# Performance work log

Hardware: AMD Instinct MI355X
Metric: run time of the kernel (lower is better)

## Reference

```python
import jax, jax.numpy as jnp
import numpy as np

K = 3  # three_nn
EPS = 1e-10


def setup_inputs() -> dict:
    key = jax.random.key(0)
    ks = jax.random.split(key, 10)
    B, N, NP = 4, 16384, 4096
    C1, C2 = 128, 256
    Cin, H1, H2, Cout = C1 + C2, 256, 256, 128
    xyz1 = jax.random.normal(ks[0], (B, N, 3), dtype=jnp.float32)
    xyz2 = jax.random.normal(ks[1], (B, NP, 3), dtype=jnp.float32)
    features1 = jax.random.normal(ks[2], (B, N, C1), dtype=jnp.float32)
    features2 = jax.random.normal(ks[3], (B, NP, C2), dtype=jnp.float32)
    def lin(k, fan_in, fan_out):
        bound = 1.0 / np.sqrt(fan_in)
        kw, kb = jax.random.split(k)
        W = jax.random.uniform(kw, (fan_in, fan_out), jnp.float32, -bound, bound)
        b = jax.random.uniform(kb, (fan_out,), jnp.float32, -bound, bound)
        return W, b
    W1, b1 = lin(ks[4], Cin, H1)
    W2, b2 = lin(ks[5], H1, H2)
    W3, b3 = lin(ks[6], H2, Cout)
    return {"xyz1": xyz1, "xyz2": xyz2, "features1": features1,
            "features2": features2, "W1": W1, "b1": b1, "W2": W2,
            "b2": b2, "W3": W3, "b3": b3}


def _three_nn(xyz1, xyz2):
    # squared pairwise distances via |a|^2 + |b|^2 - 2 a.b  -> [B, N, npoint]
    sq1 = jnp.sum(xyz1 * xyz1, axis=-1)  # [B, N]
    sq2 = jnp.sum(xyz2 * xyz2, axis=-1)  # [B, npoint]
    dots = jnp.einsum("bnd,bmd->bnm", xyz1, xyz2)
    sqdist = sq1[:, :, None] + sq2[:, None, :] - 2.0 * dots
    neg_d, idx = jax.lax.top_k(-sqdist, K)  # 3 smallest squared distances
    return -neg_d, idx  # dist:[B,N,3], idx:[B,N,3]


def reference(xyz1, xyz2, features1, features2, W1, b1, W2, b2, W3, b3):
    B = xyz1.shape[0]
    dist, idx = _three_nn(xyz1, xyz2)
    # torch custom three_nn is non-differentiable in dist
    dist = jax.lax.stop_gradient(dist)
    dist = jnp.maximum(dist, EPS)
    recip = 1.0 / dist                                  # [B, N, 3]
    weight = recip / jnp.sum(recip, axis=-1, keepdims=True)
    # three_interpolate: gather neighbor features and weighted-sum
    batch_idx = jnp.arange(B)[:, None, None]
    gathered = features2[batch_idx, idx]                # [B, N, 3, C2]
    interp = jnp.einsum("bnkc,bnk->bnc", gathered, weight)
    new_features = jnp.concatenate([features1, interp], axis=-1)
    h = jax.nn.relu(new_features @ W1 + b1)
    h = jax.nn.relu(h @ W2 + b2)
    return h @ W3 + b3
```

## Files before the change

kernel.cpp:

```cpp
#include <hip/hip_runtime.h>
#include <stdint.h>

#define QT   65536
#define NPTS 4096
#define C1   128
#define C2   256
#define CIN  384
#define COUT 128

typedef _Float16 f16;
typedef __attribute__((ext_vector_type(8))) _Float16 f16x8;
typedef __attribute__((ext_vector_type(4))) float f32x4;

__device__ __attribute__((aligned(16))) f16 g_w1p[12 * 16 * 64 * 8];
__device__ __attribute__((aligned(16))) f16 g_w2p[8 * 16 * 64 * 8];
__device__ __attribute__((aligned(16))) f16 g_w3p[8 * 8 * 64 * 8];

__device__ inline void packW(const float* __restrict__ W, f16* __restrict__ dst,
                             int i, int N, int NCB) {
  const int r = i & 63;
  const int cbk = i >> 6;
  const int cb = cbk % NCB, kcb = cbk / NCB;
  const int col = cb * 16 + (r & 15);
  const int k0 = kcb * 32 + (r >> 4) * 8;
  f16* o = dst + (size_t)i * 8;
#pragma unroll
  for (int e = 0; e < 8; ++e) o[e] = (f16)W[(size_t)(k0 + e) * N + col];
}

__global__ __launch_bounds__(256) void prep(
    const float* __restrict__ W1, const float* __restrict__ W2,
    const float* __restrict__ W3) {
  const int tid = blockIdx.x * 256 + threadIdx.x;
  const int nthr = gridDim.x * 256;
  for (int i = tid; i < 12 * 16 * 64; i += nthr) packW(W1, g_w1p, i, 256, 16);
  for (int i = tid; i < 8 * 16 * 64; i += nthr) packW(W2, g_w2p, i, 256, 16);
  for (int i = tid; i < 8 * 8 * 64; i += nthr) packW(W3, g_w3p, i, 128, 8);
}

__device__ inline uint32_t umin(uint32_t a, uint32_t b) { return a < b ? a : b; }
__device__ inline uint32_t med3u(uint32_t a, uint32_t b, uint32_t c) {
  uint32_t d;
  asm("v_med3_u32 %0, %1, %2, %3" : "=v"(d) : "v"(a), "v"(b), "v"(c));
  return d;
}

#define XS_STRIDE 392
#define HS_STRIDE 264
#define WV_OFF 50176
#define IV_OFF 51200
#define SMEM_BYTES 52224

__global__ __launch_bounds__(512) void fused_fp(
    const float* __restrict__ xyz1, const float* __restrict__ xyz2,
    const float* __restrict__ f1,   const float* __restrict__ f2,
    const float* __restrict__ W1,   const float* __restrict__ b1,
    const float* __restrict__ W2,   const float* __restrict__ b2,
    const float* __restrict__ W3,   const float* __restrict__ b3,
    float* __restrict__ out)
{
  __shared__ __align__(16) char smem[SMEM_BYTES];
  float4*   cand = (float4*)smem;
  uint32_t* mgU  = (uint32_t*)(smem + 16384);
  float*    wvp  = (float*)(smem + WV_OFF);
  int*      ivp  = (int*)(smem + IV_OFF);
  f16*      Xs   = (f16*)smem;
  f16*      Hs   = (f16*)smem;

  const int t = threadIdx.x;
  const int r = t & 63;
  const int w = t >> 6;
  const int qb = blockIdx.x * 64;
  const int batch = qb >> 14;
  const float* xz2b = xyz2 + (size_t)batch * NPTS * 3;
  const float* f2b  = f2   + (size_t)batch * NPTS * C2;

  const int q = qb + r;
  const float qx = xyz1[q * 3], qy = xyz1[q * 3 + 1], qz = xyz1[q * 3 + 2];
  const float nx = -2.f * qx, ny = -2.f * qy, nz = -2.f * qz;
  const float sq1q = qx * qx + qy * qy + qz * qz;

  uint32_t k0 = ~0u, k1 = ~0u, k2 = ~0u, k3 = ~0u, k4 = ~0u;

  auto ins5 = [&](uint32_t c) {
    uint32_t n0 = umin(k0, c);
    uint32_t n1 = med3u(k0, k1, c);
    uint32_t n2 = med3u(k1, k2, c);
    uint32_t n3 = med3u(k2, k3, c);
    uint32_t n4 = med3u(k3, k4, c);
    k0 = n0; k1 = n1; k2 = n2; k3 = n3; k4 = n4;
  };
  auto packk = [&](float e, uint32_t idx) -> uint32_t {
    e = fmaxf(e, 0.f);
    return (__builtin_bit_cast(uint32_t, e) & 0xFFFFF000u) | idx;
  };

  for (int pass = 0; pass < 4; ++pass) {
    __syncthreads();
    #pragma unroll
    for (int i = 0; i < 2; ++i) {
      int ci = t + 512 * i;
      const float* p = xz2b + (size_t)(pass * 1024 + ci) * 3;
      float x = p[0], y = p[1], z = p[2];
      cand[ci] = make_float4(x, y, z, x * x + y * y + z * z);
    }
    __syncthreads();
    const float4* cc = cand + w * 128;
    const uint32_t abase = (uint32_t)(pass * 1024 + w * 128);
    for (int m = 0; m < 128; m += 4) {
      float4 c0 = cc[m], c1 = cc[m + 1], c2 = cc[m + 2], c3 = cc[m + 3];
      float e0 = fmaf(nx, c0.x, fmaf(ny, c0.y, fmaf(nz, c0.z, c0.w))) + sq1q;
      float e1 = fmaf(nx, c1.x, fmaf(ny, c1.y, fmaf(nz, c1.z, c1.w))) + sq1q;
      float e2 = fmaf(nx, c2.x, fmaf(ny, c2.y, fmaf(nz, c2.z, c2.w))) + sq1q;
      float e3 = fmaf(nx, c3.x, fmaf(ny, c3.y, fmaf(nz, c3.z, c3.w))) + sq1q;
      ins5(packk(e0, abase + m));
      ins5(packk(e1, abase + m + 1));
      ins5(packk(e2, abase + m + 2));
      ins5(packk(e3, abase + m + 3));
    }
  }
  if (w > 0) {
    int base = ((w - 1) * 64 + r) * 5;
    mgU[base]     = k0;
    mgU[base + 1] = k1;
    mgU[base + 2] = k2;
    mgU[base + 3] = k3;
    mgU[base + 4] = k4;
  }
  __syncthreads();

  if (w == 0) {
    const double x1 = (double)qx, y1 = (double)qy, z1 = (double)qz;
    const double sq1 = x1 * x1 + y1 * y1 + z1 * z1;
    double d0 = 1e300, d1 = 1e300, d2 = 1e300;
    int j0 = 0, j1 = 0, j2 = 0;
    uint32_t surv[40];
    surv[0] = k0; surv[1] = k1; surv[2] = k2; surv[3] = k3; surv[4] = k4;
    #pragma unroll
    for (int wi = 0; wi < 7; ++wi)
      #pragma unroll
      for (int s = 0; s < 5; ++s)
        surv[5 + wi * 5 + s] = mgU[(wi * 64 + r) * 5 + s];
    #pragma unroll
    for (int s = 0; s < 40; ++s) {
      int idx = (int)(surv[s] & (NPTS - 1));
      const float* p2 = xz2b + (size_t)idx * 3;
      double x2 = (double)p2[0], y2 = (double)p2[1], z2 = (double)p2[2];
      double d = sq1 + (x2 * x2 + y2 * y2 + z2 * z2)
                     - 2.0 * (x1 * x2 + y1 * y2 + z1 * z2);
      bool c2 = (d < d2) || (d == d2 && idx < j2);
      bool c1 = (d < d1) || (d == d1 && idx < j1);
      bool c0 = (d < d0) || (d == d0 && idx < j0);
      d2 = c1 ? d1 : (c2 ? d : d2);  j2 = c1 ? j1 : (c2 ? idx : j2);
      d1 = c0 ? d0 : (c1 ? d : d1);  j1 = c0 ? j0 : (c1 ? idx : j1);
      d0 = c0 ? d : d0;              j0 = c0 ? idx : j0;
    }
    float e0 = fmaxf((float)d0, 1e-10f);
    float e1 = fmaxf((float)d1, 1e-10f);
    float e2 = fmaxf((float)d2, 1e-10f);
    float r0 = 1.f / e0, r1 = 1.f / e1, r2 = 1.f / e2;
    float inv = 1.f / (r0 + r1 + r2);
    wvp[r * 4 + 0] = r0 * inv; wvp[r * 4 + 1] = r1 * inv;
    wvp[r * 4 + 2] = r2 * inv; wvp[r * 4 + 3] = 0.f;
    ivp[r * 4 + 0] = j0; ivp[r * 4 + 1] = j1; ivp[r * 4 + 2] = j2; ivp[r * 4 + 3] = 0;
  }
  __syncthreads();

  {
    const int row = t >> 3, c = t & 7;
    f16* xr = Xs + row * XS_STRIDE;
    {
      const float* f1r = f1 + (size_t)(qb + row) * C1 + c * 16;
      float4 u0 = *(const float4*)(f1r);
      float4 u1 = *(const float4*)(f1r + 4);
      float4 u2 = *(const float4*)(f1r + 8);
      float4 u3 = *(const float4*)(f1r + 12);
      f16x8 o0, o1;
      o0[0] = (f16)u0.x; o0[1] = (f16)u0.y; o0[2] = (f16)u0.z; o0[3] = (f16)u0.w;
      o0[4] = (f16)u1.x; o0[5] = (f16)u1.y; o0[6] = (f16)u1.z; o0[7] = (f16)u1.w;
      o1[0] = (f16)u2.x; o1[1] = (f16)u2.y; o1[2] = (f16)u2.z; o1[3] = (f16)u2.w;
      o1[4] = (f16)u3.x; o1[5] = (f16)u3.y; o1[6] = (f16)u3.z; o1[7] = (f16)u3.w;
      *(f16x8*)(xr + c * 16)     = o0;
      *(f16x8*)(xr + c * 16 + 8) = o1;
    }
    const float w0 = wvp[row * 4 + 0], w1 = wvp[row * 4 + 1], w2 = wvp[row * 4 + 2];
    const float* p0 = f2b + (size_t)(ivp[row * 4 + 0] & (NPTS - 1)) * C2;
    const float* p1 = f2b + (size_t)(ivp[row * 4 + 1] & (NPTS - 1)) * C2;
    const float* p2 = f2b + (size_t)(ivp[row * 4 + 2] & (NPTS - 1)) * C2;
    #pragma unroll
    for (int ch = 0; ch < 4; ++ch) {
      const int col = ch * 64 + c * 8;
      float4 a0 = *(const float4*)(p0 + col), b0 = *(const float4*)(p0 + col + 4);
      float4 a1 = *(const float4*)(p1 + col), b1v = *(const float4*)(p1 + col + 4);
      float4 a2 = *(const float4*)(p2 + col), b2v = *(const float4*)(p2 + col + 4);
      f16x8 o;
      o[0] = (f16)(w0 * a0.x + w1 * a1.x + w2 * a2.x);
      o[1] = (f16)(w0 * a0.y + w1 * a1.y + w2 * a2.y);
      o[2] = (f16)(w0 * a0.z + w1 * a1.z + w2 * a2.z);
      o[3] = (f16)(w0 * a0.w + w1 * a1.w + w2 * a2.w);
      o[4] = (f16)(w0 * b0.x + w1 * b1v.x + w2 * b2v.x);
      o[5] = (f16)(w0 * b0.y + w1 * b1v.y + w2 * b2v.y);
      o[6] = (f16)(w0 * b0.z + w1 * b1v.z + w2 * b2v.z);
      o[7] = (f16)(w0 * b0.w + w1 * b1v.w + w2 * b2v.w);
      *(f16x8*)(xr + C1 + col) = o;
    }
  }
  __syncthreads();

  const int l16 = r & 15, quad = r >> 4;
  const int nb = w * 32;

  f32x4 acc[4][2];
  #pragma unroll
  for (int i = 0; i < 4; ++i)
    #pragma unroll
    for (int j = 0; j < 2; ++j) acc[i][j] = f32x4{0.f, 0.f, 0.f, 0.f};

  #pragma unroll
  for (int kc = 0; kc < CIN; kc += 32) {
    f16x8 a[4];
    #pragma unroll
    for (int i = 0; i < 4; ++i)
      a[i] = *(const f16x8*)(Xs + (i * 16 + l16) * XS_STRIDE + kc + quad * 8);
    f16x8 b[2];
    #pragma unroll
    for (int j = 0; j < 2; ++j)
      b[j] = *((const f16x8*)g_w1p +
               (size_t)((kc >> 5) * 16 + (w * 2 + j)) * 64 + r);
    #pragma unroll
    for (int i = 0; i < 4; ++i)
      #pragma unroll
      for (int j = 0; j < 2; ++j)
        acc[i][j] = __builtin_amdgcn_mfma_f32_16x16x32_f16(a[i], b[j], acc[i][j], 0, 0, 0);
  }
  __syncthreads();
  #pragma unroll
  for (int j = 0; j < 2; ++j) {
    float bv = b1[nb + j * 16 + l16];
    #pragma unroll
    for (int i = 0; i < 4; ++i)
      #pragma unroll
      for (int e = 0; e < 4; ++e) {
        int row = i * 16 + quad * 4 + e;
        Hs[row * HS_STRIDE + nb + j * 16 + l16] =
            (f16)fmaxf(acc[i][j][e] + bv, 0.f);
      }
  }
  __syncthreads();

  f32x4 acc2[4][2];
  #pragma unroll
  for (int i = 0; i < 4; ++i)
    #pragma unroll
    for (int j = 0; j < 2; ++j) acc2[i][j] = f32x4{0.f, 0.f, 0.f, 0.f};

  #pragma unroll
  for (int kc = 0; kc < 256; kc += 32) {
    f16x8 a[4];
    #pragma unroll
    for (int i = 0; i < 4; ++i)
      a[i] = *(const f16x8*)(Hs + (i * 16 + l16) * HS_STRIDE + kc + quad * 8);
    f16x8 b[2];
    #pragma unroll
    for (int j = 0; j < 2; ++j)
      b[j] = *((const f16x8*)g_w2p +
               (size_t)((kc >> 5) * 16 + (w * 2 + j)) * 64 + r);
    #pragma unroll
    for (int i = 0; i < 4; ++i)
      #pragma unroll
      for (int j = 0; j < 2; ++j)
        acc2[i][j] = __builtin_amdgcn_mfma_f32_16x16x32_f16(a[i], b[j], acc2[i][j], 0, 0, 0);
  }
  __syncthreads();
  #pragma unroll
  for (int j = 0; j < 2; ++j) {
    float bv = b2[nb + j * 16 + l16];
    #pragma unroll
    for (int i = 0; i < 4; ++i)
      #pragma unroll
      for (int e = 0; e < 4; ++e) {
        int row = i * 16 + quad * 4 + e;
        Hs[row * HS_STRIDE + nb + j * 16 + l16] =
            (f16)fmaxf(acc2[i][j][e] + bv, 0.f);
      }
  }
  __syncthreads();

  const int nb3 = w * 16;
  f32x4 acc3[4];
  #pragma unroll
  for (int i = 0; i < 4; ++i) acc3[i] = f32x4{0.f, 0.f, 0.f, 0.f};

  #pragma unroll
  for (int kc = 0; kc < 256; kc += 32) {
    f16x8 a[4];
    #pragma unroll
    for (int i = 0; i < 4; ++i)
      a[i] = *(const f16x8*)(Hs + (i * 16 + l16) * HS_STRIDE + kc + quad * 8);
    f16x8 b;
    b = *((const f16x8*)g_w3p + (size_t)((kc >> 5) * 8 + w) * 64 + r);
    #pragma unroll
    for (int i = 0; i < 4; ++i)
      acc3[i] = __builtin_amdgcn_mfma_f32_16x16x32_f16(a[i], b, acc3[i], 0, 0, 0);
  }
  {
    int col = nb3 + l16;
    float bv = b3[col];
    #pragma unroll
    for (int i = 0; i < 4; ++i)
      #pragma unroll
      for (int e = 0; e < 4; ++e) {
        int row = i * 16 + quad * 4 + e;
        out[(size_t)(qb + row) * COUT + col] = acc3[i][e] + bv;
      }
  }
}

extern "C" void kernel_launch(void* const* d_in, const int* in_sizes, int n_in,
                              void* d_out, int out_size, void* d_ws, size_t ws_size,
                              hipStream_t stream)
{
  (void)out_size; (void)d_ws; (void)ws_size;
  static const int expect[10] = {196608, 49152, 8388608, 4194304,
                                 98304, 256, 65536, 256, 32768, 128};
  const void* p[10];
  bool ok = (n_in == 10);
  if (ok) {
    bool used[10] = {false};
    for (int e = 0; e < 10; ++e) {
      p[e] = nullptr;
      for (int i = 0; i < 10; ++i) {
        if (!used[i] && in_sizes[i] == expect[e]) {
          p[e] = d_in[i]; used[i] = true; break;
        }
      }
      if (!p[e]) { ok = false; break; }
    }
  }
  if (!ok)
    for (int e = 0; e < 10; ++e) p[e] = d_in[e < n_in ? e : (n_in - 1)];

  prep<<<96, 256, 0, stream>>>(
      (const float*)p[4], (const float*)p[6], (const float*)p[8]);

  fused_fp<<<QT / 64, 512, 0, stream>>>(
      (const float*)p[0], (const float*)p[1],
      (const float*)p[2], (const float*)p[3],
      (const float*)p[4], (const float*)p[5],
      (const float*)p[6], (const float*)p[7],
      (const float*)p[8], (const float*)p[9],
      (float*)d_out);
}
```

Baseline: 226.1 us.

## Precompute xyz2 candidates globally and stream them per wave instead of LDS staging

The prep kernel now builds a global float4 table of candidate points with precomputed squared norms. The fused kernel drops its four-pass LDS staging, along with the barriers around it. Each wave instead reads a contiguous 512-candidate slice straight from global memory with a wave-uniform address, so the loads can go through scalar or broadcast paths. Weight packing is also vectorized with float4 reads and f16x8 writes, and the prep grid grows to 256 blocks. The cost is more global or cache traffic per wave in place of LDS reuse.

```diff
diff --git a/kernel.cpp b/kernel.cpp
--- a/kernel.cpp
+++ b/kernel.cpp
@@ -15,27 +15,38 @@
 __device__ __attribute__((aligned(16))) f16 g_w1p[12 * 16 * 64 * 8];
 __device__ __attribute__((aligned(16))) f16 g_w2p[8 * 16 * 64 * 8];
 __device__ __attribute__((aligned(16))) f16 g_w3p[8 * 8 * 64 * 8];
-
-__device__ inline void packW(const float* __restrict__ W, f16* __restrict__ dst,
-                             int i, int N, int NCB) {
-  const int r = i & 63;
-  const int cbk = i >> 6;
+__device__ __attribute__((aligned(16))) float4 g_cand[4 * NPTS];
+
+__device__ inline void packW4(const float* __restrict__ W, f16* __restrict__ dst,
+                              int i, int N, int NCB) {
+  const int g = i & 3, quad = (i >> 2) & 3, cbk = i >> 4;
   const int cb = cbk % NCB, kcb = cbk / NCB;
-  const int col = cb * 16 + (r & 15);
-  const int k0 = kcb * 32 + (r >> 4) * 8;
-  f16* o = dst + (size_t)i * 8;
+  const int col = cb * 16 + g * 4;
+  const int k0 = kcb * 32 + quad * 8;
+  f16x8 o[4];
 #pragma unroll
-  for (int e = 0; e < 8; ++e) o[e] = (f16)W[(size_t)(k0 + e) * N + col];
+  for (int e = 0; e < 8; ++e) {
+    float4 v = *(const float4*)(W + (size_t)(k0 + e) * N + col);
+    o[0][e] = (f16)v.x; o[1][e] = (f16)v.y; o[2][e] = (f16)v.z; o[3][e] = (f16)v.w;
+  }
+  f16* base = dst + ((size_t)cbk * 64 + quad * 16 + g * 4) * 8;
+#pragma unroll
+  for (int j = 0; j < 4; ++j) *(f16x8*)(base + j * 8) = o[j];
 }
 
 __global__ __launch_bounds__(256) void prep(
-    const float* __restrict__ W1, const float* __restrict__ W2,
-    const float* __restrict__ W3) {
+    const float* __restrict__ xyz2, const float* __restrict__ W1,
+    const float* __restrict__ W2,   const float* __restrict__ W3) {
   const int tid = blockIdx.x * 256 + threadIdx.x;
   const int nthr = gridDim.x * 256;
-  for (int i = tid; i < 12 * 16 * 64; i += nthr) packW(W1, g_w1p, i, 256, 16);
-  for (int i = tid; i < 8 * 16 * 64; i += nthr) packW(W2, g_w2p, i, 256, 16);
-  for (int i = tid; i < 8 * 8 * 64; i += nthr) packW(W3, g_w3p, i, 128, 8);
+  for (int i = tid; i < 4 * NPTS; i += nthr) {
+    const float* p = xyz2 + (size_t)i * 3;
+    float x = p[0], y = p[1], z = p[2];
+    g_cand[i] = make_float4(x, y, z, fmaf(x, x, fmaf(y, y, z * z)));
+  }
+  for (int i = tid; i < 12 * 16 * 16; i += nthr) packW4(W1, g_w1p, i, 256, 16);
+  for (int i = tid; i < 8 * 16 * 16; i += nthr) packW4(W2, g_w2p, i, 256, 16);
+  for (int i = tid; i < 8 * 8 * 16; i += nthr) packW4(W3, g_w3p, i, 128, 8);
 }
 
 __device__ inline uint32_t umin(uint32_t a, uint32_t b) { return a < b ? a : b; }
@@ -60,7 +71,6 @@
     float* __restrict__ out)
 {
   __shared__ __align__(16) char smem[SMEM_BYTES];
-  float4*   cand = (float4*)smem;
   uint32_t* mgU  = (uint32_t*)(smem + 16384);
   float*    wvp  = (float*)(smem + WV_OFF);
   int*      ivp  = (int*)(smem + IV_OFF);
@@ -95,20 +105,13 @@
     return (__builtin_bit_cast(uint32_t, e) & 0xFFFFF000u) | idx;
   };
 
-  for (int pass = 0; pass < 4; ++pass) {
-    __syncthreads();
-    #pragma unroll
-    for (int i = 0; i < 2; ++i) {
-      int ci = t + 512 * i;
-      const float* p = xz2b + (size_t)(pass * 1024 + ci) * 3;
-      float x = p[0], y = p[1], z = p[2];
-      cand[ci] = make_float4(x, y, z, x * x + y * y + z * z);
-    }
-    __syncthreads();
-    const float4* cc = cand + w * 128;
-    const uint32_t abase = (uint32_t)(pass * 1024 + w * 128);
-    for (int m = 0; m < 128; m += 4) {
-      float4 c0 = cc[m], c1 = cc[m + 1], c2 = cc[m + 2], c3 = cc[m + 3];
+  {
+    const int wu = __builtin_amdgcn_readfirstlane(w);
+    const float4* __restrict__ cp = g_cand + (batch << 12) + (wu << 9);
+    const uint32_t abase = (uint32_t)(wu << 9);
+    #pragma unroll 2
+    for (int m = 0; m < 512; m += 4) {
+      float4 c0 = cp[m], c1 = cp[m + 1], c2 = cp[m + 2], c3 = cp[m + 3];
       float e0 = fmaf(nx, c0.x, fmaf(ny, c0.y, fmaf(nz, c0.z, c0.w))) + sq1q;
       float e1 = fmaf(nx, c1.x, fmaf(ny, c1.y, fmaf(nz, c1.z, c1.w))) + sq1q;
       float e2 = fmaf(nx, c2.x, fmaf(ny, c2.y, fmaf(nz, c2.z, c2.w))) + sq1q;
@@ -119,6 +122,7 @@
       ins5(packk(e3, abase + m + 3));
     }
   }
+
   if (w > 0) {
     int base = ((w - 1) * 64 + r) * 5;
     mgU[base]     = k0;
@@ -340,8 +344,9 @@
   if (!ok)
     for (int e = 0; e < 10; ++e) p[e] = d_in[e < n_in ? e : (n_in - 1)];
 
-  prep<<<96, 256, 0, stream>>>(
-      (const float*)p[4], (const float*)p[6], (const float*)p[8]);
+  prep<<<256, 256, 0, stream>>>(
+      (const float*)p[1], (const float*)p[4],
+      (const float*)p[6], (const float*)p[8]);
 
   fused_fp<<<QT / 64, 512, 0, stream>>>(
       (const float*)p[0], (const float*)p[1],
```

After: 225.9 us. About the same (-0.1%).
